# Kernel optimization log

Measured on AMD Instinct MI355X. Metric: run time of the kernel, lower is better.

Reference implementation:

```python
import jax, jax.numpy as jnp
import numpy as np

B = 1
E = 8388608                      # embedding size (dim 1)
NNZ = 131072                     # inhibition links
MIN_SPARSITY = 0.002
MAX_SPARSITY = 0.02
BOOST_PERCENT = 1e-8             # forward default boost_percent
MAX_ACTIVE = int(np.ceil(MAX_SPARSITY * E))    # 167773, torch uses .item() -> static
MIN_ACTIVE = int(np.floor(MIN_SPARSITY * E))   # 16777


def setup_inputs() -> dict:
    key = jax.random.key(0)
    k1, k3, k4, k5 = jax.random.split(key, 4)
    x = jax.random.normal(k1, (B, E, 1, 1), dtype=jnp.float32)
    boost_tensor = jnp.zeros((B, E, 1, 1), dtype=jnp.float32)   # initial boost state (zeros_like in module)
    inh_affector = jax.random.randint(k3, (NNZ,), 0, E, dtype=jnp.int32)
    inh_affectee = jax.random.randint(k4, (NNZ,), 0, E, dtype=jnp.int32)
    # inhibition values are negative (self-inhibition, affect_value=-0.01 scale)
    inh_values = -jax.random.uniform(k5, (NNZ,), dtype=jnp.float32) * 0.05
    return {"x": x, "boost_tensor": boost_tensor, "inh_values": inh_values,
            "inh_affector": inh_affector, "inh_affectee": inh_affectee}


def reference(x, boost_tensor, inh_values, inh_affector, inh_affectee):
    xf = x.reshape(B, E)
    bf = boost_tensor.reshape(B, E)

    # --- run_boosting: PercentClosenessBoosting (units far from max get boosted) ---
    boost_new = bf + (1.0 - xf / jnp.max(xf)) * jnp.float32(BOOST_PERCENT)
    boosted = jnp.maximum(xf, 0.0) + boost_new   # tensor_above + boost_tensor

    # --- apply_sparse_self_affector: tens[affectee] += tens[affector] * values ---
    # RHS gathered from the pre-update tensor, scatter-add onto affectee coords.
    inhibited = boosted.at[0, inh_affectee].add(boosted[0, inh_affector] * inh_values)

    # --- run_k_winners_positive: keep top max_active per row, binarize positives ---
    topv, topi = jax.lax.top_k(inhibited, MAX_ACTIVE)          # [B, K]
    rows = jnp.arange(B)[:, None]
    result = jnp.zeros((B, E), dtype=jnp.float32).at[rows, topi].set(
        (topv > 0).astype(jnp.float32))

    # --- choose_boosted_to_satisfy_minimum ---
    actually_active = jnp.sum(result)
    _, boost_idx = jax.lax.top_k(boost_new, MIN_ACTIVE)        # [B, MIN_ACTIVE]
    to_activate = jnp.ceil(jnp.float32(MIN_ACTIVE) - actually_active)
    need = actually_active < jnp.float32(MIN_ACTIVE)
    add = need & (jnp.arange(MIN_ACTIVE, dtype=jnp.float32) < to_activate)
    add = jnp.broadcast_to(add.astype(jnp.float32), (B, MIN_ACTIVE))
    out = result.at[rows, boost_idx].max(add)

    return out.reshape(B, E, 1, 1)
```

## Files before the change

### kernel.cpp

```cpp
#include <hip/hip_runtime.h>
#include <stdint.h>

#define E_SIZE   8388608
#define N4       (E_SIZE / 4)
#define NNZ_SZ   131072
#define K_ACT    167773
#define MIN_ACT  16777
#define CAP      262144
#define BCAP     2048
#define TINY_F   9.5367431640625e-7f
#define NBINS    16384
#define SHIFT1   18

__device__ __forceinline__ unsigned int f2A(float f) {
    unsigned int u = __float_as_uint(f);
    return (u & 0x80000000u) ? ~u : (u | 0x80000000u);
}
__device__ __forceinline__ unsigned int f2D(float f) { return ~f2A(f); }
__device__ __forceinline__ float A2f(unsigned int A) {
    unsigned int u = (A & 0x80000000u) ? (A & 0x7FFFFFFFu) : ~A;
    return __uint_as_float(u);
}
__device__ __forceinline__ float D2f(unsigned int D) { return A2f(~D); }

__device__ __forceinline__ float boostedf(float v, float b, float mx) {
    return fmaxf(v, 0.0f) + (b + (1.0f - v / mx) * 1e-8f);
}
__device__ __forceinline__ unsigned int binclamp14(float v) {
    return (v < TINY_F) ? (NBINS - 1u) : (f2D(v) >> SHIFT1);
}

__device__ void block_select(const unsigned int* counts, int nbins, unsigned int Krem,
                             unsigned int* res, unsigned int* scratch) {
    int t = threadIdx.x;
    int per = nbins >> 10; if (per == 0) per = 1;
    int nth = nbins / per;
    unsigned int part = 0;
    if (t < nth)
        for (int j = 0; j < per; j++) part += counts[t * per + j];
    scratch[t] = part;
    unsigned int ws = part;
    for (int off = 32; off; off >>= 1) ws += __shfl_down(ws, off, 64);
    if ((t & 63) == 0) scratch[1024 + (t >> 6)] = ws;
    __syncthreads();
    if (t == 0) {
        unsigned int cum = 0;
        int w = 0;
        for (; w < 15; w++) {
            unsigned int s = scratch[1024 + w];
            if (cum + s >= Krem) break;
            cum += s;
        }
        int tt = w * 64, te = tt + 63;
        for (; tt < te; tt++) {
            unsigned int s = scratch[tt];
            if (cum + s >= Krem) break;
            cum += s;
        }
        int b = tt * per, be = b + per - 1;
        for (; b < be; b++) {
            unsigned int s = counts[b];
            if (cum + s >= Krem) break;
            cum += s;
        }
        res[0] = (unsigned int)b;
        res[1] = Krem - cum;
    }
    __syncthreads();
}

__global__ void __launch_bounds__(256)
k_max(const float4* __restrict__ x, unsigned int* __restrict__ pmax,
      unsigned int* __restrict__ ctrl, unsigned int* __restrict__ hist,
      float4* __restrict__ accum) {
    int t = threadIdx.x, blk = blockIdx.x;
    if (blk == 0 && t < 64) ctrl[t] = 0u;
    if (t < 16) hist[blk * 16 + t] = 0u;
    int tid = blk * 256 + t;
    unsigned int m = 0u;
    const float4 z4 = make_float4(0.f, 0.f, 0.f, 0.f);
    for (int i = tid; i < N4; i += 1024 * 256) {
        float4 v = x[i];
        accum[i] = z4;
        m = max(m, f2A(v.x)); m = max(m, f2A(v.y));
        m = max(m, f2A(v.z)); m = max(m, f2A(v.w));
    }
    for (int off = 32; off; off >>= 1)
        m = max(m, __shfl_down(m, off, 64));
    __shared__ unsigned int sm[4];
    if ((t & 63) == 0) sm[t >> 6] = m;
    __syncthreads();
    if (t == 0) pmax[blk] = max(max(sm[0], sm[1]), max(sm[2], sm[3]));
}

__device__ __forceinline__ float reduce_pmax(const unsigned int* __restrict__ pmax,
                                             unsigned int* smax) {
    int t = threadIdx.x;
    unsigned int m = pmax[t];
    for (int off = 32; off; off >>= 1)
        m = max(m, __shfl_down(m, off, 64));
    if ((t & 63) == 0) smax[t >> 6] = m;
    __syncthreads();
    if (t == 0) {
        unsigned int r = smax[0];
        for (int i = 1; i < 16; i++) r = max(r, smax[i]);
        smax[0] = r;
    }
    __syncthreads();
    return A2f(smax[0]);
}

__device__ __forceinline__ float reduce_pmax256(const unsigned int* __restrict__ pmax,
                                                unsigned int* smax) {
    int t = threadIdx.x;
    unsigned int m = max(max(pmax[t], pmax[t + 256]),
                         max(pmax[t + 512], pmax[t + 768]));
    for (int off = 32; off; off >>= 1)
        m = max(m, __shfl_down(m, off, 64));
    if ((t & 63) == 0) smax[t >> 6] = m;
    __syncthreads();
    if (t == 0) smax[0] = max(max(smax[0], smax[1]), max(smax[2], smax[3]));
    __syncthreads();
    return A2f(smax[0]);
}

__global__ void __launch_bounds__(256)
k_scatter(const float* __restrict__ x, const float* __restrict__ bf,
          const float* __restrict__ vals, const int* __restrict__ aff,
          const int* __restrict__ afe, float* __restrict__ accum,
          const unsigned int* __restrict__ pmax) {
    __shared__ unsigned int smax[16];
    float mx = reduce_pmax256(pmax, smax);
    int i = blockIdx.x * 256 + threadIdx.x;
    int a = aff[i], e = afe[i];
    float bo = boostedf(x[a], bf[a], mx);
    atomicAdd(&accum[e], bo * vals[i]);
}

__global__ void __launch_bounds__(1024)
k_boost_hist(const float4* __restrict__ x, const float4* __restrict__ bf,
             const float4* __restrict__ acc, float4* __restrict__ out,
             const unsigned int* __restrict__ pmax, unsigned int* __restrict__ hist) {
    __shared__ unsigned int h[NBINS];
    __shared__ unsigned int smax[16];
    float mx = reduce_pmax(pmax, smax);
    int t = threadIdx.x;
    for (int i = t; i < NBINS; i += 1024) h[i] = 0u;
    __syncthreads();
    unsigned int tiny = 0;
    int gtid = blockIdx.x * 1024 + t;
    for (int i = gtid; i < N4; i += 256 * 1024) {
        float4 v = x[i], b = bf[i], a = acc[i];
        float4 r;
        r.x = boostedf(v.x, b.x, mx) + a.x;
        r.y = boostedf(v.y, b.y, mx) + a.y;
        r.z = boostedf(v.z, b.z, mx) + a.z;
        r.w = boostedf(v.w, b.w, mx) + a.w;
        out[i] = r;
        #define HISTONE(c) { if ((c) < TINY_F) tiny++; \
            else atomicAdd(&h[f2D(c) >> SHIFT1], 1u); }
        HISTONE(r.x); HISTONE(r.y); HISTONE(r.z); HISTONE(r.w);
        #undef HISTONE
    }
    for (int off = 32; off; off >>= 1)
        tiny += __shfl_down(tiny, off, 64);
    if ((t & 63) == 0 && tiny) atomicAdd(&h[NBINS - 1], tiny);
    __syncthreads();
    for (int k = t; k < NBINS; k += 1024) {
        unsigned int c = h[k];
        if (c) atomicAdd(&hist[k], c);
    }
}

__global__ void __launch_bounds__(1024)
k_markscan(float4* __restrict__ out, const unsigned int* __restrict__ hist,
           unsigned int* __restrict__ ctrl, unsigned int* __restrict__ gidx,
           unsigned int* __restrict__ gD) {
    __shared__ unsigned int scratch[1040];
    __shared__ unsigned int res[2];
    __shared__ unsigned int cidx[BCAP];
    __shared__ unsigned int cDs[BCAP];
    __shared__ unsigned int scnt, sbase;
    int t = threadIdx.x;
    block_select(hist, NBINS, (unsigned int)K_ACT, res, scratch);
    unsigned int b1 = res[0];
    if (t == 0) {
        scnt = 0;
        if (blockIdx.x == 0) {
            atomicExch(&ctrl[32], res[0]);
            atomicExch(&ctrl[33], res[1]);
        }
    }
    __syncthreads();
    int gtid = blockIdx.x * 1024 + t;
    for (int i = gtid; i < N4; i += 512 * 1024) {
        float4 f = out[i];
        float4 r;
        #define MARKONE(c, rr, comp) { \
            unsigned int bc = binclamp14(c); \
            if (bc < b1) rr = ((c) > 0.0f) ? 1.0f : 0.0f; \
            else { rr = 0.0f; if (bc == b1) { \
                unsigned int p = atomicAdd(&scnt, 1u); \
                if (p < BCAP) { cidx[p] = (unsigned int)i * 4u + comp; cDs[p] = f2D(c); } } } }
        MARKONE(f.x, r.x, 0u); MARKONE(f.y, r.y, 1u);
        MARKONE(f.z, r.z, 2u); MARKONE(f.w, r.w, 3u);
        #undef MARKONE
        out[i] = r;
    }
    __syncthreads();
    if (t == 0) {
        unsigned int m = min(scnt, (unsigned int)BCAP);
        scnt = m;
        sbase = atomicAdd(&ctrl[7], m);
    }
    __syncthreads();
    unsigned int m = scnt, base = sbase;
    for (unsigned int i = t; i < m; i += 1024) {
        unsigned int g = base + i;
        if (g < CAP) { gidx[g] = cidx[i]; gD[g] = cDs[i]; }
    }
}

__global__ void __launch_bounds__(1024)
k_select(float* __restrict__ out, const unsigned int* __restrict__ ctrl,
         const unsigned int* __restrict__ gidx, const unsigned int* __restrict__ gD) {
    __shared__ unsigned int h512[512];
    __shared__ unsigned int scratch[1040];
    __shared__ unsigned int res[2];
    __shared__ unsigned int ties[128];
    __shared__ unsigned int tcnt;
    int t = threadIdx.x;
    unsigned int nc = min(ctrl[7], (unsigned int)CAP);
    unsigned int b1 = ctrl[32];
    unsigned int Krem = ctrl[33];

    if (t < 512) h512[t] = 0u;
    if (t == 0) tcnt = 0u;
    __syncthreads();
    for (unsigned int i = t; i < nc; i += 1024)
        atomicAdd(&h512[(gD[i] >> 9) & 511u], 1u);
    __syncthreads();
    block_select(h512, 512, Krem, res, scratch);
    unsigned int b2 = res[0], Krem2 = res[1];

    if (t < 512) h512[t] = 0u;
    __syncthreads();
    for (unsigned int i = t; i < nc; i += 1024) {
        unsigned int D = gD[i];
        if (((D >> 9) & 511u) == b2) atomicAdd(&h512[D & 511u], 1u);
    }
    __syncthreads();
    block_select(h512, 512, Krem2, res, scratch);
    unsigned int b3 = res[0], need = res[1];
    unsigned int T = (b1 << SHIFT1) | (b2 << 9) | b3;

    for (unsigned int i = t; i < nc; i += 1024) {
        if (gD[i] == T) {
            unsigned int p = atomicAdd(&tcnt, 1u);
            if (p < 128) ties[p] = gidx[i];
        }
    }
    __syncthreads();
    unsigned int M = min(tcnt, 128u);
    float val = (D2f(T) > 0.0f) ? 1.0f : 0.0f;
    for (unsigned int i = t; i < M; i += 1024) {
        unsigned int idx = ties[i];
        unsigned int rank = 0;
        for (unsigned int j = 0; j < M; j++) rank += (ties[j] < idx) ? 1u : 0u;
        if (rank < need) out[idx] = val;
    }
    for (unsigned int i = t; i < nc; i += 1024) {
        unsigned int D = gD[i];
        if (D < T) out[gidx[i]] = (D2f(D) > 0.0f) ? 1.0f : 0.0f;
    }
}

extern "C" void kernel_launch(void* const* d_in, const int* in_sizes, int n_in,
                              void* d_out, int out_size, void* d_ws, size_t ws_size,
                              hipStream_t stream) {
    const float* x    = (const float*)d_in[0];
    const float* bf   = (const float*)d_in[1];
    const float* vals = (const float*)d_in[2];
    const int*   aff  = (const int*)d_in[3];
    const int*   afe  = (const int*)d_in[4];
    float* out = (float*)d_out;

    unsigned int* ctrl = (unsigned int*)d_ws;
    unsigned int* pmax = (unsigned int*)((char*)d_ws + 4096);
    unsigned int* hist = (unsigned int*)((char*)d_ws + 8192);
    unsigned int* gidx = (unsigned int*)((char*)d_ws + 8192 + (size_t)NBINS * 4);
    unsigned int* gD   = (unsigned int*)((char*)d_ws + 8192 + (size_t)NBINS * 4 + (size_t)CAP * 4);
    float* accum = (float*)((char*)d_ws + (size_t)(4 << 20));

    k_max<<<1024, 256, 0, stream>>>((const float4*)x, pmax, ctrl, hist, (float4*)accum);
    k_scatter<<<512, 256, 0, stream>>>(x, bf, vals, aff, afe, accum, pmax);
    k_boost_hist<<<256, 1024, 0, stream>>>((const float4*)x, (const float4*)bf,
                                           (const float4*)accum, (float4*)out, pmax, hist);
    k_markscan<<<512, 1024, 0, stream>>>((float4*)out, hist, ctrl, gidx, gD);
    k_select<<<1, 1024, 0, stream>>>(out, ctrl, gidx, gD);
}
```

Before: 193.8 us.

## Scatter-add directly into output, drop accum buffer, split boost and histogram passes

Removes the separate zero-initialised accumulation buffer. A new pass writes the boosted values straight to the output, the inhibition atomics then add into the output, and a separate histogram pass re-reads it. This avoids zeroing one full-size buffer and reading it back, so less DRAM traffic. The cost is an extra kernel launch and a second read of the output, which may be served from the large last-level cache. The histogram pass also uses twice as many blocks, so more per-bin global atomics. The single-block select kernel now stages candidate keys in LDS so its repeated scans avoid global memory.

New measurement: 187.8 us. 3.1% less time.

```diff
diff --git a/kernel.cpp b/kernel.cpp
--- a/kernel.cpp
+++ b/kernel.cpp
@@ -11,6 +11,7 @@
 #define TINY_F   9.5367431640625e-7f
 #define NBINS    16384
 #define SHIFT1   18
+#define SEL_LDS  32768
 
 __device__ __forceinline__ unsigned int f2A(float f) {
     unsigned int u = __float_as_uint(f);
@@ -71,17 +72,14 @@
 
 __global__ void __launch_bounds__(256)
 k_max(const float4* __restrict__ x, unsigned int* __restrict__ pmax,
-      unsigned int* __restrict__ ctrl, unsigned int* __restrict__ hist,
-      float4* __restrict__ accum) {
+      unsigned int* __restrict__ ctrl, unsigned int* __restrict__ hist) {
     int t = threadIdx.x, blk = blockIdx.x;
     if (blk == 0 && t < 64) ctrl[t] = 0u;
     if (t < 16) hist[blk * 16 + t] = 0u;
     int tid = blk * 256 + t;
     unsigned int m = 0u;
-    const float4 z4 = make_float4(0.f, 0.f, 0.f, 0.f);
     for (int i = tid; i < N4; i += 1024 * 256) {
         float4 v = x[i];
-        accum[i] = z4;
         m = max(m, f2A(v.x)); m = max(m, f2A(v.y));
         m = max(m, f2A(v.z)); m = max(m, f2A(v.w));
     }
@@ -124,39 +122,46 @@
     return A2f(smax[0]);
 }
 
+__global__ void __launch_bounds__(1024)
+k_boost(const float4* __restrict__ x, const float4* __restrict__ bf,
+        float4* __restrict__ out, const unsigned int* __restrict__ pmax) {
+    __shared__ unsigned int smax[16];
+    float mx = reduce_pmax(pmax, smax);
+    int gtid = blockIdx.x * 1024 + threadIdx.x;
+    for (int i = gtid; i < N4; i += 512 * 1024) {
+        float4 v = x[i], b = bf[i];
+        float4 r;
+        r.x = boostedf(v.x, b.x, mx);
+        r.y = boostedf(v.y, b.y, mx);
+        r.z = boostedf(v.z, b.z, mx);
+        r.w = boostedf(v.w, b.w, mx);
+        out[i] = r;
+    }
+}
+
 __global__ void __launch_bounds__(256)
 k_scatter(const float* __restrict__ x, const float* __restrict__ bf,
           const float* __restrict__ vals, const int* __restrict__ aff,
-          const int* __restrict__ afe, float* __restrict__ accum,
+          const int* __restrict__ afe, float* __restrict__ out,
           const unsigned int* __restrict__ pmax) {
     __shared__ unsigned int smax[16];
     float mx = reduce_pmax256(pmax, smax);
     int i = blockIdx.x * 256 + threadIdx.x;
     int a = aff[i], e = afe[i];
     float bo = boostedf(x[a], bf[a], mx);
-    atomicAdd(&accum[e], bo * vals[i]);
+    atomicAdd(&out[e], bo * vals[i]);
 }
 
 __global__ void __launch_bounds__(1024)
-k_boost_hist(const float4* __restrict__ x, const float4* __restrict__ bf,
-             const float4* __restrict__ acc, float4* __restrict__ out,
-             const unsigned int* __restrict__ pmax, unsigned int* __restrict__ hist) {
+k_hist(const float4* __restrict__ out, unsigned int* __restrict__ hist) {
     __shared__ unsigned int h[NBINS];
-    __shared__ unsigned int smax[16];
-    float mx = reduce_pmax(pmax, smax);
     int t = threadIdx.x;
     for (int i = t; i < NBINS; i += 1024) h[i] = 0u;
     __syncthreads();
     unsigned int tiny = 0;
     int gtid = blockIdx.x * 1024 + t;
-    for (int i = gtid; i < N4; i += 256 * 1024) {
-        float4 v = x[i], b = bf[i], a = acc[i];
-        float4 r;
-        r.x = boostedf(v.x, b.x, mx) + a.x;
-        r.y = boostedf(v.y, b.y, mx) + a.y;
-        r.z = boostedf(v.z, b.z, mx) + a.z;
-        r.w = boostedf(v.w, b.w, mx) + a.w;
-        out[i] = r;
+    for (int i = gtid; i < N4; i += 512 * 1024) {
+        float4 r = out[i];
         #define HISTONE(c) { if ((c) < TINY_F) tiny++; \
             else atomicAdd(&h[f2D(c) >> SHIFT1], 1u); }
         HISTONE(r.x); HISTONE(r.y); HISTONE(r.z); HISTONE(r.w);
@@ -224,6 +229,7 @@
 __global__ void __launch_bounds__(1024)
 k_select(float* __restrict__ out, const unsigned int* __restrict__ ctrl,
          const unsigned int* __restrict__ gidx, const unsigned int* __restrict__ gD) {
+    __shared__ unsigned int sD[SEL_LDS];
     __shared__ unsigned int h512[512];
     __shared__ unsigned int scratch[1040];
     __shared__ unsigned int res[2];
@@ -233,12 +239,16 @@
     unsigned int nc = min(ctrl[7], (unsigned int)CAP);
     unsigned int b1 = ctrl[32];
     unsigned int Krem = ctrl[33];
-
+    unsigned int ns = min(nc, (unsigned int)SEL_LDS);
+
+    for (unsigned int i = t; i < ns; i += 1024) sD[i] = gD[i];
     if (t < 512) h512[t] = 0u;
     if (t == 0) tcnt = 0u;
     __syncthreads();
+    #define GETD(i) (((i) < ns) ? sD[(i)] : gD[(i)])
+
     for (unsigned int i = t; i < nc; i += 1024)
-        atomicAdd(&h512[(gD[i] >> 9) & 511u], 1u);
+        atomicAdd(&h512[(GETD(i) >> 9) & 511u], 1u);
     __syncthreads();
     block_select(h512, 512, Krem, res, scratch);
     unsigned int b2 = res[0], Krem2 = res[1];
@@ -246,7 +256,7 @@
     if (t < 512) h512[t] = 0u;
     __syncthreads();
     for (unsigned int i = t; i < nc; i += 1024) {
-        unsigned int D = gD[i];
+        unsigned int D = GETD(i);
         if (((D >> 9) & 511u) == b2) atomicAdd(&h512[D & 511u], 1u);
     }
     __syncthreads();
@@ -255,7 +265,7 @@
     unsigned int T = (b1 << SHIFT1) | (b2 << 9) | b3;
 
     for (unsigned int i = t; i < nc; i += 1024) {
-        if (gD[i] == T) {
+        if (GETD(i) == T) {
             unsigned int p = atomicAdd(&tcnt, 1u);
             if (p < 128) ties[p] = gidx[i];
         }
@@ -270,9 +280,10 @@
         if (rank < need) out[idx] = val;
     }
     for (unsigned int i = t; i < nc; i += 1024) {
-        unsigned int D = gD[i];
+        unsigned int D = GETD(i);
         if (D < T) out[gidx[i]] = (D2f(D) > 0.0f) ? 1.0f : 0.0f;
     }
+    #undef GETD
 }
 
 extern "C" void kernel_launch(void* const* d_in, const int* in_sizes, int n_in,
@@ -290,12 +301,12 @@
     unsigned int* hist = (unsigned int*)((char*)d_ws + 8192);
     unsigned int* gidx = (unsigned int*)((char*)d_ws + 8192 + (size_t)NBINS * 4);
     unsigned int* gD   = (unsigned int*)((char*)d_ws + 8192 + (size_t)NBINS * 4 + (size_t)CAP * 4);
-    float* accum = (float*)((char*)d_ws + (size_t)(4 << 20));
-
-    k_max<<<1024, 256, 0, stream>>>((const float4*)x, pmax, ctrl, hist, (float4*)accum);
-    k_scatter<<<512, 256, 0, stream>>>(x, bf, vals, aff, afe, accum, pmax);
-    k_boost_hist<<<256, 1024, 0, stream>>>((const float4*)x, (const float4*)bf,
-                                           (const float4*)accum, (float4*)out, pmax, hist);
+
+    k_max<<<1024, 256, 0, stream>>>((const float4*)x, pmax, ctrl, hist);
+    k_boost<<<512, 1024, 0, stream>>>((const float4*)x, (const float4*)bf,
+                                      (float4*)out, pmax);
+    k_scatter<<<512, 256, 0, stream>>>(x, bf, vals, aff, afe, out, pmax);
+    k_hist<<<512, 1024, 0, stream>>>((const float4*)out, hist);
     k_markscan<<<512, 1024, 0, stream>>>((float4*)out, hist, ctrl, gidx, gD);
     k_select<<<1, 1024, 0, stream>>>(out, ctrl, gidx, gD);
 }
```
